# Kernel tuning notes

Measured on AMD Instinct MI355X. Metric: run time of the kernel, lower is better.

Reference implementation:

```python
import jax, jax.numpy as jnp
import numpy as np

B, N = 8192, 4096
P = Q = R = S = 64            # square Monarch blocks: sqrt(N)
K = N // P                    # 64
L = N * Q // (P * R)          # 64


def setup_inputs() -> dict:
    key = jax.random.key(0)
    kx, k1, k2 = jax.random.split(key, 3)
    x = jax.random.normal(kx, (B, N), dtype=jnp.float32)
    w1_bfly = jax.random.normal(k1, (K, Q, P), dtype=jnp.float32)
    w2_bfly = jax.random.normal(k2, (L, S, R), dtype=jnp.float32)
    return {"x": x, "w1_bfly": w1_bfly, "w2_bfly": w2_bfly}


def reference(x, w1_bfly, w2_bfly):
    # x: (B, n); w1: (k, q, p); w2: (l, s, r); k*p = n, l*r = k*q
    b, n = x.shape
    k, q, p = w1_bfly.shape
    l, s, r = w2_bfly.shape
    # stage 1: block-diagonal bmm -> (b, k, q)
    out1 = jnp.einsum('bkp,kqp->bkq', x.reshape(b, k, p), w1_bfly)
    # permutation between stages: (b, k*q) -> (b, r, l) -> (b, l, r)
    out1 = out1.reshape(b, r, l).transpose(0, 2, 1)
    # stage 2: block-diagonal bmm -> (b, l, s)
    out2 = jnp.einsum('blr,lsr->bls', out1, w2_bfly)
    # final permute: (b, l, s) -> (b, s, l) -> (b, s*l)
    return out2.transpose(0, 2, 1).reshape(b, s * l)
```

## Files before the change

kernel.cpp:

```cpp
#include <hip/hip_runtime.h>


typedef __bf16 bf16x8 __attribute__((ext_vector_type(8)));
typedef float  float4v __attribute__((ext_vector_type(4)));

__global__ __launch_bounds__(256)
void cvt_weights(const float* __restrict__ w1, const float* __restrict__ w2,
                 __bf16* __restrict__ wb) {
    const int i = (blockIdx.x * 256 + threadIdx.x) * 8;
    float4v a = *(const float4v*)(w1 + i);
    float4v b = *(const float4v*)(w1 + i + 4);
    bf16x8 v;
    v[0]=(__bf16)a[0]; v[1]=(__bf16)a[1]; v[2]=(__bf16)a[2]; v[3]=(__bf16)a[3];
    v[4]=(__bf16)b[0]; v[5]=(__bf16)b[1]; v[6]=(__bf16)b[2]; v[7]=(__bf16)b[3];
    *(bf16x8*)(wb + i) = v;
    a = *(const float4v*)(w2 + i);
    b = *(const float4v*)(w2 + i + 4);
    v[0]=(__bf16)a[0]; v[1]=(__bf16)a[1]; v[2]=(__bf16)a[2]; v[3]=(__bf16)a[3];
    v[4]=(__bf16)b[0]; v[5]=(__bf16)b[1]; v[6]=(__bf16)b[2]; v[7]=(__bf16)b[3];
    *(bf16x8*)(wb + 262144 + i) = v;
}

__global__ __launch_bounds__(512, 2)
void monarch_fused(const float* __restrict__ x,
                   const __bf16* __restrict__ w1b,
                   const __bf16* __restrict__ w2b,
                   float* __restrict__ out)
{
    __shared__ __align__(16) __bf16 Y[16 * 16 * 64];

    const int tid  = threadIdx.x;
    const int wid  = tid >> 6;
    const int lane = tid & 63;
    const int m    = lane & 15;
    const int quad = lane >> 4;
    const int b0   = blockIdx.x * 16;

    bf16x8 xa[8][2];
    {
        const float* xp = x + (long)(b0 + m) * 4096 + wid * 512 + quad * 8;
        #pragma unroll
        for (int j = 0; j < 8; ++j) {
            #pragma unroll
            for (int h = 0; h < 2; ++h) {
                float4v lo = *(const float4v*)(xp + j * 64 + h * 32);
                float4v hi = *(const float4v*)(xp + j * 64 + h * 32 + 4);
                bf16x8 v;
                v[0]=(__bf16)lo[0]; v[1]=(__bf16)lo[1]; v[2]=(__bf16)lo[2]; v[3]=(__bf16)lo[3];
                v[4]=(__bf16)hi[0]; v[5]=(__bf16)hi[1]; v[6]=(__bf16)hi[2]; v[7]=(__bf16)hi[3];
                xa[j][h] = v;
            }
        }
    }

    const int lg = wid >> 1;
    const int sh = wid & 1;

    for (int qc = 0; qc < 4; ++qc) {
        float4v acc[8];
        #pragma unroll
        for (int j = 0; j < 8; ++j) {
            const int k = wid * 8 + j;
            const __bf16* w1p = w1b + ((k * 64 + qc * 16 + m) * 64) + quad * 8;
            bf16x8 bb0 = *(const bf16x8*)(w1p);
            bf16x8 bb1 = *(const bf16x8*)(w1p + 32);
            float4v c = {0.f, 0.f, 0.f, 0.f};
            c = __builtin_amdgcn_mfma_f32_16x16x32_bf16(xa[j][0], bb0, c, 0, 0, 0);
            c = __builtin_amdgcn_mfma_f32_16x16x32_bf16(xa[j][1], bb1, c, 0, 0, 0);
            acc[j] = c;
        }

        __syncthreads();

        #pragma unroll
        for (int reg = 0; reg < 4; ++reg) {
            const int bl = quad * 4 + reg;
            const int cs = wid ^ (m & 7) ^ (bl & 7);
            bf16x8 v;
            #pragma unroll
            for (int j = 0; j < 8; ++j) v[j] = (__bf16)acc[j][reg];
            *(bf16x8*)(&Y[((bl * 16 + m) * 8 + cs) * 8]) = v;
        }
        __syncthreads();

        float4v acc2[4][2];
        #pragma unroll
        for (int li = 0; li < 4; ++li)
            #pragma unroll
            for (int st = 0; st < 2; ++st) acc2[li][st] = (float4v){0.f, 0.f, 0.f, 0.f};

        #pragma unroll
        for (int h = 0; h < 2; ++h) {
            #pragma unroll
            for (int li = 0; li < 4; ++li) {
                const int ll = lg * 4 + li;
                const int l  = qc * 16 + ll;
                const int kc = h * 4 + quad;
                const int cs = kc ^ (ll & 7) ^ (m & 7);
                bf16x8 a2 = *(const bf16x8*)(&Y[((m * 16 + ll) * 8 + cs) * 8]);
                const __bf16* w2p = w2b + (l * 64) * 64 + h * 32 + quad * 8;
                #pragma unroll
                for (int st = 0; st < 2; ++st) {
                    const int s = (sh * 2 + st) * 16 + m;
                    bf16x8 b2 = *(const bf16x8*)(w2p + s * 64);
                    acc2[li][st] = __builtin_amdgcn_mfma_f32_16x16x32_bf16(a2, b2, acc2[li][st], 0, 0, 0);
                }
            }
        }

        #pragma unroll
        for (int st = 0; st < 2; ++st) {
            #pragma unroll
            for (int reg = 0; reg < 4; ++reg) {
                float4v v;
                #pragma unroll
                for (int li = 0; li < 4; ++li) v[li] = acc2[li][st][reg];
                float* dst = out + (long)(b0 + quad * 4 + reg) * 4096
                                 + ((sh * 2 + st) * 16 + m) * 64 + qc * 16 + lg * 4;
                *(float4v*)dst = v;
            }
        }
    }
}

extern "C" void kernel_launch(void* const* d_in, const int* in_sizes, int n_in,
                              void* d_out, int out_size, void* d_ws, size_t ws_size,
                              hipStream_t stream) {
    const float* x  = (const float*)d_in[0];
    const float* w1 = (const float*)d_in[1];
    const float* w2 = (const float*)d_in[2];
    float* out = (float*)d_out;
    __bf16* wb = (__bf16*)d_ws;

    hipLaunchKernelGGL(cvt_weights, dim3(128), dim3(256), 0, stream, w1, w2, wb);
    hipLaunchKernelGGL(monarch_fused, dim3(8192 / 16), dim3(512), 0, stream,
                       x, wb, wb + 262144, out);
}
```

Baseline: 339.6 us.

## Use 1024-thread blocks with full-tile LDS staging and coalesced output writes

The fused Monarch kernel moves to 1024-thread blocks. Each block computes its whole stage-1 tile (all q chunks) into a 128 KB dynamic LDS buffer, instead of looping over four q chunks with a barrier pair per chunk. Stage 2 then runs once over 16 l-blocks per wave, and the outputs are staged through the same LDS in two halves so global stores write contiguous rows. This cuts barrier count and makes output writes coalesced. In exchange it needs very large LDS, one resident block per CU, and a tight launch-bounds request that may cap registers and cause spills.

```diff
diff --git a/kernel.cpp b/kernel.cpp
--- a/kernel.cpp
+++ b/kernel.cpp
@@ -21,13 +21,15 @@
     *(bf16x8*)(wb + 262144 + i) = v;
 }
 
-__global__ __launch_bounds__(512, 2)
+__global__ __launch_bounds__(1024, 4)
 void monarch_fused(const float* __restrict__ x,
                    const __bf16* __restrict__ w1b,
                    const __bf16* __restrict__ w2b,
                    float* __restrict__ out)
 {
-    __shared__ __align__(16) __bf16 Y[16 * 16 * 64];
+    extern __shared__ __align__(16) unsigned char smem[];
+    __bf16* Y = (__bf16*)smem;
+    float*  O = (float*)smem;
 
     const int tid  = threadIdx.x;
     const int wid  = tid >> 6;
@@ -36,9 +38,12 @@
     const int quad = lane >> 4;
     const int b0   = blockIdx.x * 16;
 
+    const int kw = wid & 7;
+    const int qh = wid >> 3;
+
     bf16x8 xa[8][2];
     {
-        const float* xp = x + (long)(b0 + m) * 4096 + wid * 512 + quad * 8;
+        const float* xp = x + (long)(b0 + m) * 4096 + kw * 512 + quad * 8;
         #pragma unroll
         for (int j = 0; j < 8; ++j) {
             #pragma unroll
@@ -53,15 +58,14 @@
         }
     }
 
-    const int lg = wid >> 1;
-    const int sh = wid & 1;
-
-    for (int qc = 0; qc < 4; ++qc) {
+    #pragma unroll
+    for (int t = 0; t < 2; ++t) {
+        const int qt = qh * 2 + t;
         float4v acc[8];
         #pragma unroll
         for (int j = 0; j < 8; ++j) {
-            const int k = wid * 8 + j;
-            const __bf16* w1p = w1b + ((k * 64 + qc * 16 + m) * 64) + quad * 8;
+            const int k = kw * 8 + j;
+            const __bf16* w1p = w1b + ((k * 64 + qt * 16 + m) * 64) + quad * 8;
             bf16x8 bb0 = *(const bf16x8*)(w1p);
             bf16x8 bb1 = *(const bf16x8*)(w1p + 32);
             float4v c = {0.f, 0.f, 0.f, 0.f};
@@ -69,56 +73,70 @@
             c = __builtin_amdgcn_mfma_f32_16x16x32_bf16(xa[j][1], bb1, c, 0, 0, 0);
             acc[j] = c;
         }
-
-        __syncthreads();
-
         #pragma unroll
         for (int reg = 0; reg < 4; ++reg) {
             const int bl = quad * 4 + reg;
-            const int cs = wid ^ (m & 7) ^ (bl & 7);
+            const int q  = qt * 16 + m;
+            const int cs = kw ^ (m & 7) ^ (bl & 7);
             bf16x8 v;
             #pragma unroll
             for (int j = 0; j < 8; ++j) v[j] = (__bf16)acc[j][reg];
-            *(bf16x8*)(&Y[((bl * 16 + m) * 8 + cs) * 8]) = v;
+            *(bf16x8*)(&Y[((bl * 64 + q) * 8 + cs) * 8]) = v;
+        }
+    }
+    __syncthreads();
+
+    const int lgrp = wid & 3;
+    const int sgrp = wid >> 2;
+    const int s    = sgrp * 16 + m;
+
+    float4v acc2[16];
+    #pragma unroll
+    for (int li = 0; li < 16; ++li) acc2[li] = (float4v){0.f, 0.f, 0.f, 0.f};
+
+    #pragma unroll
+    for (int h = 0; h < 2; ++h) {
+        #pragma unroll
+        for (int li = 0; li < 16; ++li) {
+            const int l   = lgrp * 16 + li;
+            const int cs2 = (h * 4 + quad) ^ (l & 7) ^ (m & 7);
+            bf16x8 a2 = *(const bf16x8*)(&Y[((m * 64 + l) * 8 + cs2) * 8]);
+            bf16x8 b2 = *(const bf16x8*)(w2b + l * 4096 + s * 64 + h * 32 + quad * 8);
+            acc2[li] = __builtin_amdgcn_mfma_f32_16x16x32_bf16(a2, b2, acc2[li], 0, 0, 0);
+        }
+    }
+    __syncthreads();
+
+    #pragma unroll
+    for (int h2 = 0; h2 < 2; ++h2) {
+        if (h2) __syncthreads();
+
+        if ((sgrp >> 1) == h2) {
+            const int so = (sgrp & 1) * 16 + m;
+            #pragma unroll
+            for (int li4 = 0; li4 < 4; ++li4) {
+                const int l4 = lgrp * 4 + li4;
+                #pragma unroll
+                for (int reg = 0; reg < 4; ++reg) {
+                    const int b    = quad * 4 + reg;
+                    const int phys = l4 ^ (so & 7) ^ (quad << 1);
+                    float4v v = { acc2[li4 * 4 + 0][reg], acc2[li4 * 4 + 1][reg],
+                                  acc2[li4 * 4 + 2][reg], acc2[li4 * 4 + 3][reg] };
+                    *(float4v*)(&O[((b * 32 + so) << 6) + (phys << 2)]) = v;
+                }
+            }
         }
         __syncthreads();
 
-        float4v acc2[4][2];
+        const int l4r = tid & 15;
+        const int sor = (tid >> 4) & 31;
         #pragma unroll
-        for (int li = 0; li < 4; ++li)
-            #pragma unroll
-            for (int st = 0; st < 2; ++st) acc2[li][st] = (float4v){0.f, 0.f, 0.f, 0.f};
-
-        #pragma unroll
-        for (int h = 0; h < 2; ++h) {
-            #pragma unroll
-            for (int li = 0; li < 4; ++li) {
-                const int ll = lg * 4 + li;
-                const int l  = qc * 16 + ll;
-                const int kc = h * 4 + quad;
-                const int cs = kc ^ (ll & 7) ^ (m & 7);
-                bf16x8 a2 = *(const bf16x8*)(&Y[((m * 16 + ll) * 8 + cs) * 8]);
-                const __bf16* w2p = w2b + (l * 64) * 64 + h * 32 + quad * 8;
-                #pragma unroll
-                for (int st = 0; st < 2; ++st) {
-                    const int s = (sh * 2 + st) * 16 + m;
-                    bf16x8 b2 = *(const bf16x8*)(w2p + s * 64);
-                    acc2[li][st] = __builtin_amdgcn_mfma_f32_16x16x32_bf16(a2, b2, acc2[li][st], 0, 0, 0);
-                }
-            }
-        }
-
-        #pragma unroll
-        for (int st = 0; st < 2; ++st) {
-            #pragma unroll
-            for (int reg = 0; reg < 4; ++reg) {
-                float4v v;
-                #pragma unroll
-                for (int li = 0; li < 4; ++li) v[li] = acc2[li][st][reg];
-                float* dst = out + (long)(b0 + quad * 4 + reg) * 4096
-                                 + ((sh * 2 + st) * 16 + m) * 64 + qc * 16 + lg * 4;
-                *(float4v*)dst = v;
-            }
+        for (int it = 0; it < 8; ++it) {
+            const int b    = it * 2 + (tid >> 9);
+            const int phys = l4r ^ (sor & 7) ^ (((b >> 2) & 3) << 1);
+            float4v v = *(const float4v*)(&O[((b * 32 + sor) << 6) + (phys << 2)]);
+            float* dst = out + (long)(b0 + b) * 4096 + (h2 * 32 + sor) * 64 + l4r * 4;
+            *(float4v*)dst = v;
         }
     }
 }
@@ -133,6 +151,6 @@
     __bf16* wb = (__bf16*)d_ws;
 
     hipLaunchKernelGGL(cvt_weights, dim3(128), dim3(256), 0, stream, w1, w2, wb);
-    hipLaunchKernelGGL(monarch_fused, dim3(8192 / 16), dim3(512), 0, stream,
+    hipLaunchKernelGGL(monarch_fused, dim3(8192 / 16), dim3(1024), 131072, stream,
                        x, wb, wb + 262144, out);
 }
```

New measurement: 300.0 us. -11.6%, faster.
